# Kernel tuning notes

Hardware: AMD Instinct MI355X
Metric: run time of the kernel (lower is better)

The kernel has to match this reference:

```python
import jax, jax.numpy as jnp
import numpy as np

B, S, D = 4, 4096, 1024
H, DH = 16, 64            # heads, head dim (D = H*DH)
W = 256                   # local window size; S % W == 0
HID = 2 * D               # GEGLU hidden dim
LN_EPS = 1e-5


def setup_inputs() -> dict:
    key = jax.random.key(0)
    ks = jax.random.split(key, 8)
    w = lambda k, shp: (jax.random.normal(k, shp, jnp.float32) * 0.02)
    return {
        "x": jax.random.normal(ks[0], (B, S, D), jnp.float32),
        "ln1_g": jnp.ones((D,), jnp.float32), "ln1_b": jnp.zeros((D,), jnp.float32),
        "ln2_g": jnp.ones((D,), jnp.float32), "ln2_b": jnp.zeros((D,), jnp.float32),
        "Wq": w(ks[1], (D, D)), "Wk": w(ks[2], (D, D)), "Wv": w(ks[3], (D, D)),
        "Wo": w(ks[4], (D, D)), "bo": jnp.zeros((D,), jnp.float32),
        "W1": w(ks[5], (D, 2 * HID)), "b1": jnp.zeros((2 * HID,), jnp.float32),
        "W2": w(ks[6], (HID, D)), "b2": jnp.zeros((D,), jnp.float32),
    }


def layer_norm(x, g, b):
    mu = jnp.mean(x, axis=-1, keepdims=True)
    var = jnp.mean(jnp.square(x - mu), axis=-1, keepdims=True)
    return (x - mu) * jax.lax.rsqrt(var + LN_EPS) * g + b


def local_causal_attention(x, Wq, Wk, Wv, Wo, bo):
    b, s, d = x.shape
    nw = s // W
    def split_heads(t):  # [b,s,d] -> [b,H,nw,W,DH]
        return t.reshape(b, s, H, DH).transpose(0, 2, 1, 3).reshape(b, H, nw, W, DH)
    q = split_heads(x @ Wq)
    k = split_heads(x @ Wk)
    v = split_heads(x @ Wv)
    # look_backward=1: each window attends to [prev window, current window]
    def with_prev(t):  # [b,H,nw,W,DH] -> [b,H,nw,2W,DH]
        prev = jnp.pad(t, ((0, 0), (0, 0), (1, 0), (0, 0), (0, 0)))[:, :, :-1]
        return jnp.concatenate([prev, t], axis=3)
    kc, vc = with_prev(k), with_prev(v)
    scores = jnp.einsum("bhnqd,bhnkd->bhnqk", q, kc) * (DH ** -0.5)
    # positions: qpos = n*W + i ; kpos = (n-1)*W + j, j in [0,2W)
    n = jnp.arange(nw)[:, None, None]
    i = jnp.arange(W)[None, :, None]
    j = jnp.arange(2 * W)[None, None, :]
    qpos = n * W + i
    kpos = (n - 1) * W + j
    mask = (kpos <= qpos) & (kpos >= 0)  # causal + left-edge padding
    scores = jnp.where(mask[None, None], scores, jnp.finfo(scores.dtype).min)
    attn = jax.nn.softmax(scores, axis=-1)
    out = jnp.einsum("bhnqk,bhnkd->bhnqd", attn, vc)
    out = out.reshape(b, H, s, DH).transpose(0, 2, 1, 3).reshape(b, s, d)
    return out @ Wo + bo


def geglu(x, W1, b1, W2, b2):
    h = x @ W1 + b1
    a, g = jnp.split(h, 2, axis=-1)
    return (a * jax.nn.gelu(g, approximate=False)) @ W2 + b2


def reference(x, ln1_g, ln1_b, ln2_g, ln2_b, Wq, Wk, Wv, Wo, bo, W1, b1, W2, b2):
    x = x + local_causal_attention(layer_norm(x, ln1_g, ln1_b), Wq, Wk, Wv, Wo, bo)
    x = x + geglu(layer_norm(x, ln2_g, ln2_b), W1, b1, W2, b2)
    return x
```

## Files before the change

kernel.cpp:

```cpp
#include <hip/hip_runtime.h>
#include <hip/hip_bf16.h>

typedef __attribute__((ext_vector_type(4))) float f32x4;
typedef __attribute__((ext_vector_type(8))) short bf16x8;
typedef __attribute__((ext_vector_type(8))) unsigned short u16x8;

static __device__ __forceinline__ ushort f2b(float f) {
  union { float f; unsigned u; } v; v.f = f;
  unsigned r = v.u + 0x7fffu + ((v.u >> 16) & 1u);
  return (ushort)(r >> 16);
}

static __device__ __forceinline__ float gelu_fast(float g) {
  const float c0 = 0.7978845608028654f, c1 = 0.044715f;
  const float u = c0 * (g + c1 * g * g * g);
  const float e = __expf(2.0f * u);
  const float t = 1.0f - 2.0f / (e + 1.0f);
  return 0.5f * g * (1.0f + t);
}

static __device__ __forceinline__ void gload_lds16(const void* g, void* l) {
  __builtin_amdgcn_global_load_lds(
      (__attribute__((address_space(1))) void*)(g),
      (__attribute__((address_space(3))) void*)(l), 16, 0, 0);
}

__global__ __launch_bounds__(256) void transpose_cast_kernel(
    const float* __restrict__ W, ushort* __restrict__ Wt, int K, int N) {
  __shared__ float tile[32][33];
  const int n0 = blockIdx.x * 32, k0 = blockIdx.y * 32;
  const int tx = threadIdx.x, ty = threadIdx.y;
#pragma unroll
  for (int r = 0; r < 32; r += 8)
    tile[ty + r][tx] = W[(size_t)(k0 + ty + r) * N + n0 + tx];
  __syncthreads();
#pragma unroll
  for (int r = 0; r < 32; r += 8)
    Wt[(size_t)(n0 + ty + r) * K + k0 + tx] = f2b(tile[tx][ty + r]);
}

__global__ __launch_bounds__(256) void ln_kernel(
    const float* __restrict__ x, const float* __restrict__ g,
    const float* __restrict__ bb, ushort* __restrict__ out) {
  const int row = blockIdx.x;
  const float* xr = x + (size_t)row * 1024;
  const float4 v = *(const float4*)&xr[threadIdx.x * 4];
  float s = v.x + v.y + v.z + v.w;
  float s2 = v.x * v.x + v.y * v.y + v.z * v.z + v.w * v.w;
#pragma unroll
  for (int off = 32; off > 0; off >>= 1) {
    s += __shfl_down(s, off);
    s2 += __shfl_down(s2, off);
  }
  __shared__ float red[8];
  const int lane = threadIdx.x & 63, wv = threadIdx.x >> 6;
  if (lane == 0) { red[wv] = s; red[4 + wv] = s2; }
  __syncthreads();
  s = red[0] + red[1] + red[2] + red[3];
  s2 = red[4] + red[5] + red[6] + red[7];
  const float mu = s * (1.0f / 1024.0f);
  const float rs = rsqrtf(s2 * (1.0f / 1024.0f) - mu * mu + 1e-5f);
  const int c = threadIdx.x * 4;
  ushort4 o;
  o.x = f2b((v.x - mu) * rs * g[c + 0] + bb[c + 0]);
  o.y = f2b((v.y - mu) * rs * g[c + 1] + bb[c + 1]);
  o.z = f2b((v.z - mu) * rs * g[c + 2] + bb[c + 2]);
  o.w = f2b((v.w - mu) * rs * g[c + 3] + bb[c + 3]);
  *(ushort4*)&out[(size_t)row * 1024 + c] = o;
}

template <int MODE>
__global__ __launch_bounds__(512) void gemm256_kernel(
    const ushort* __restrict__ A, const ushort* __restrict__ Bt,
    const int M, const int N, const int K,
    ushort* __restrict__ Cb, float* __restrict__ Cf,
    const float* __restrict__ bias, const float* __restrict__ res) {
  __shared__ __align__(16) ushort lds[3 * 16384];

  const int ntn = N >> 8;
  const int bn = blockIdx.x % ntn;
  const int bm = blockIdx.x / ntn;
  const int tid = threadIdx.x;
  const int l = tid & 63, w = tid >> 6;
  const int wm = w >> 2, wn = w & 3;
  const int fr = l & 15, fq = l >> 4;

  const ushort* Ab = A + (size_t)bm * 256 * K;
  const ushort* Bb = Bt + (size_t)bn * 256 * K;

  const int srow = (l >> 2);
  const int scol = (((l & 3) ^ ((l >> 2) & 3)) * 8);

  f32x4 acc[8][4];
#pragma unroll
  for (int m = 0; m < 8; m++)
#pragma unroll
    for (int n = 0; n < 4; n++) acc[m][n] = (f32x4)0.0f;

  const int NT = K >> 5;

#define STAGE256(t)                                                            \
  {                                                                            \
    const int b3 = (t) % 3;                                                    \
    const size_t kk = (size_t)(t) * 32;                                        \
    _Pragma("unroll") for (int i = 0; i < 2; i++) {                            \
      const int r = (w * 2 + i) * 16 + srow;                                   \
      gload_lds16(Ab + (size_t)r * K + kk + scol,                              \
                  &lds[b3 * 16384 + (w * 2 + i) * 512]);                       \
      gload_lds16(Bb + (size_t)r * K + kk + scol,                              \
                  &lds[b3 * 16384 + 8192 + (w * 2 + i) * 512]);                \
    }                                                                          \
  }

  STAGE256(0);
  STAGE256(1);

  for (int t = 0; t < NT; ++t) {
    if (t + 2 < NT) {
      STAGE256(t + 2);
      asm volatile("s_waitcnt vmcnt(8)" ::: "memory");
    } else if (t + 1 < NT) {
      asm volatile("s_waitcnt vmcnt(4)" ::: "memory");
    } else {
      asm volatile("s_waitcnt vmcnt(0)" ::: "memory");
    }
    __builtin_amdgcn_s_barrier();
    asm volatile("" ::: "memory");

    const ushort* La = &lds[(t % 3) * 16384];
    const ushort* Lb = La + 8192;

    bf16x8 af[8], bf[4];
#pragma unroll
    for (int m = 0; m < 8; m++) {
      const int r = wm * 128 + m * 16 + fr;
      af[m] = *(const bf16x8*)&La[r * 32 + ((fq ^ (r & 3)) * 8)];
    }
#pragma unroll
    for (int n = 0; n < 4; n++) {
      const int r = wn * 64 + n * 16 + fr;
      bf[n] = *(const bf16x8*)&Lb[r * 32 + ((fq ^ (r & 3)) * 8)];
    }

    __builtin_amdgcn_s_setprio(1);
#pragma unroll
    for (int m = 0; m < 8; m++)
#pragma unroll
      for (int n = 0; n < 4; n++)
        acc[m][n] = __builtin_amdgcn_mfma_f32_16x16x32_bf16(af[m], bf[n], acc[m][n], 0, 0, 0);
    __builtin_amdgcn_s_setprio(0);

    asm volatile("" ::: "memory");
    __builtin_amdgcn_s_barrier();
  }
#undef STAGE256

  const int rowb = bm * 256 + wm * 128 + fq * 4;
  const int colb = bn * 256 + wn * 64 + fr;
#pragma unroll
  for (int m = 0; m < 8; m++) {
#pragma unroll
    for (int n = 0; n < 4; n++) {
      const int col = colb + n * 16;
#pragma unroll
      for (int j = 0; j < 4; j++) {
        const int row = rowb + m * 16 + j;
        float vv = acc[m][n][j];
        if (MODE == 0) {
          Cb[(size_t)row * N + col] = f2b(vv);
        } else if (MODE == 2) {
          if (col < 1024) vv *= 0.125f;
          Cb[(size_t)row * N + col] = f2b(vv);
        } else {
          Cf[(size_t)row * N + col] = vv + bias[col] + res[(size_t)row * N + col];
        }
      }
    }
  }
}

__global__ __launch_bounds__(256) void gemm_geglu_kernel(
    const ushort* __restrict__ A, const ushort* __restrict__ W1t,
    const float* __restrict__ b1, ushort* __restrict__ U) {
  const int K = 1024;
  __shared__ __align__(16) ushort lsA[128 * 32];
  __shared__ __align__(16) ushort lsBa[64 * 32];
  __shared__ __align__(16) ushort lsBg[64 * 32];
  const int bn = blockIdx.x & 31;
  const int bm = blockIdx.x >> 5;
  const int tid = threadIdx.x;
  const int lane = tid & 63, wv = tid >> 6;
  const int wr = wv >> 1, wc = wv & 1;
  const int fr = lane & 15, fq = lane >> 4;

  f32x4 acca[4][2], accg[4][2];
#pragma unroll
  for (int m = 0; m < 4; m++)
#pragma unroll
    for (int nn = 0; nn < 2; nn++) { acca[m][nn] = (f32x4)0.0f; accg[m][nn] = (f32x4)0.0f; }

  const ushort* Ab = A + (size_t)bm * 128 * K;
  const ushort* Bab = W1t + (size_t)bn * 64 * K;
  const ushort* Bgb = W1t + (size_t)(2048 + bn * 64) * K;
  const int r0 = tid >> 2;
  const int cseg = (tid & 3) * 8;

  for (int k0 = 0; k0 < K; k0 += 32) {
    gload_lds16(Ab + (size_t)r0 * K + (k0 + cseg), &lsA[wv * 512]);
    gload_lds16(Ab + (size_t)(r0 + 64) * K + (k0 + cseg), &lsA[wv * 512 + 2048]);
    gload_lds16(Bab + (size_t)r0 * K + (k0 + cseg), &lsBa[wv * 512]);
    gload_lds16(Bgb + (size_t)r0 * K + (k0 + cseg), &lsBg[wv * 512]);
    __syncthreads();
    bf16x8 af[4], ba[2], bg[2];
#pragma unroll
    for (int m = 0; m < 4; m++)
      af[m] = *(const bf16x8*)&lsA[(wr * 64 + m * 16 + fr) * 32 + fq * 8];
#pragma unroll
    for (int nn = 0; nn < 2; nn++) {
      ba[nn] = *(const bf16x8*)&lsBa[(wc * 32 + nn * 16 + fr) * 32 + fq * 8];
      bg[nn] = *(const bf16x8*)&lsBg[(wc * 32 + nn * 16 + fr) * 32 + fq * 8];
    }
#pragma unroll
    for (int m = 0; m < 4; m++)
#pragma unroll
      for (int nn = 0; nn < 2; nn++) {
        acca[m][nn] = __builtin_amdgcn_mfma_f32_16x16x32_bf16(af[m], ba[nn], acca[m][nn], 0, 0, 0);
        accg[m][nn] = __builtin_amdgcn_mfma_f32_16x16x32_bf16(af[m], bg[nn], accg[m][nn], 0, 0, 0);
      }
    __syncthreads();
  }

  const int rowb = bm * 128 + wr * 64 + fq * 4;
  const int colb = bn * 64 + wc * 32 + fr;
#pragma unroll
  for (int m = 0; m < 4; m++) {
#pragma unroll
    for (int nn = 0; nn < 2; nn++) {
      const int col = colb + nn * 16;
      const float b1a = b1[col];
      const float b1g = b1[2048 + col];
#pragma unroll
      for (int j = 0; j < 4; j++) {
        const int row = rowb + m * 16 + j;
        const float a = acca[m][nn][j] + b1a;
        const float gg = accg[m][nn][j] + b1g;
        U[(size_t)row * 2048 + col] = f2b(a * gelu_fast(gg));
      }
    }
  }
}

__global__ __launch_bounds__(256, 3) void attn_kernel(
    const ushort* __restrict__ Q, const ushort* __restrict__ Kb,
    const ushort* __restrict__ Vb, ushort* __restrict__ O, const int qs) {
  const int bx = blockIdx.x;
  const int n = bx & 15;
  const int h = (bx >> 4) & 15;
  const int b = bx >> 8;
  const int tid = threadIdx.x;
  const int lane = tid & 63, wv = tid >> 6;
  const int fr = lane & 15, fq = lane >> 4;

  __shared__ __align__(16) ushort Kl[64 * 72];
  __shared__ __align__(16) ushort Vt[64 * 70];
  __shared__ __align__(16) ushort Pl[4][64 * 68];

  const size_t qrow0 = (size_t)b * 4096 + (size_t)n * 256;

  bf16x8 qf[4][2];
#pragma unroll
  for (int m = 0; m < 4; m++)
#pragma unroll
    for (int kh = 0; kh < 2; kh++)
      qf[m][kh] = *(const bf16x8*)&Q[(qrow0 + wv * 64 + m * 16 + fr) * qs + h * 64 + kh * 32 + fq * 8];

  f32x4 oacc[4][4];
#pragma unroll
  for (int m = 0; m < 4; m++)
#pragma unroll
    for (int d = 0; d < 4; d++) oacc[m][d] = (f32x4)0.0f;

  float lsum[4][4];
#pragma unroll
  for (int m = 0; m < 4; m++)
#pragma unroll
    for (int j = 0; j < 4; j++) lsum[m][j] = 0.0f;

  const int c0 = (n == 0) ? 4 : 0;
  for (int c = c0; c < 8; c++) {
    const size_t kvrow0 =
        (size_t)((long long)b * 4096 + (long long)n * 256 + (long long)c * 64 - 256);
#pragma unroll
    for (int p = 0; p < 2; p++) {
      const int s = tid + p * 256;
      const int rr = s >> 3, cs2 = s & 7;
      *(u16x8*)&Kl[rr * 72 + cs2 * 8] =
          *(const u16x8*)&Kb[(kvrow0 + rr) * qs + h * 64 + cs2 * 8];
      const u16x8 vvv = *(const u16x8*)&Vb[(kvrow0 + rr) * qs + h * 64 + cs2 * 8];
#pragma unroll
      for (int i = 0; i < 8; i++) Vt[(cs2 * 8 + i) * 70 + rr] = vvv[i];
    }
    __syncthreads();

    if (c <= wv + 4) {
      const bool diag = (c == wv + 4);
#pragma unroll
      for (int nn = 0; nn < 4; nn++) {
        f32x4 sa[4];
#pragma unroll
        for (int m = 0; m < 4; m++) sa[m] = (f32x4)0.0f;
#pragma unroll
        for (int kh = 0; kh < 2; kh++) {
          const bf16x8 bk = *(const bf16x8*)&Kl[(nn * 16 + fr) * 72 + kh * 32 + fq * 8];
#pragma unroll
          for (int m = 0; m < 4; m++)
            sa[m] = __builtin_amdgcn_mfma_f32_16x16x32_bf16(qf[m][kh], bk, sa[m], 0, 0, 0);
        }
#pragma unroll
        for (int m = 0; m < 4; m++)
#pragma unroll
          for (int j = 0; j < 4; j++) {
            float p = __expf(sa[m][j]);
            if (diag && (nn * 16 + fr > m * 16 + fq * 4 + j)) p = 0.0f;
            lsum[m][j] += p;
            Pl[wv][(m * 16 + fq * 4 + j) * 68 + nn * 16 + fr] = f2b(p);
          }
      }
      __builtin_amdgcn_s_setprio(1);
#pragma unroll
      for (int kh = 0; kh < 2; kh++) {
        bf16x8 pa[4];
#pragma unroll
        for (int m = 0; m < 4; m++)
          pa[m] = *(const bf16x8*)&Pl[wv][(m * 16 + fr) * 68 + kh * 32 + fq * 8];
#pragma unroll
        for (int d = 0; d < 4; d++) {
          const bf16x8 vb = *(const bf16x8*)&Vt[(d * 16 + fr) * 70 + kh * 32 + fq * 8];
#pragma unroll
          for (int m = 0; m < 4; m++)
            oacc[m][d] = __builtin_amdgcn_mfma_f32_16x16x32_bf16(pa[m], vb, oacc[m][d], 0, 0, 0);
        }
      }
      __builtin_amdgcn_s_setprio(0);
    }
    __syncthreads();
  }

  float rl[4][4];
#pragma unroll
  for (int m = 0; m < 4; m++)
#pragma unroll
    for (int j = 0; j < 4; j++) {
      float t = lsum[m][j];
      t += __shfl_xor(t, 1);
      t += __shfl_xor(t, 2);
      t += __shfl_xor(t, 4);
      t += __shfl_xor(t, 8);
      rl[m][j] = 1.0f / t;
    }

#pragma unroll
  for (int m = 0; m < 4; m++)
#pragma unroll
    for (int d = 0; d < 4; d++)
#pragma unroll
      for (int j = 0; j < 4; j++) {
        const float o = oacc[m][d][j] * rl[m][j];
        O[(qrow0 + wv * 64 + m * 16 + fq * 4 + j) * 1024 + h * 64 + d * 16 + fr] = f2b(o);
      }
}

extern "C" void kernel_launch(void* const* d_in, const int* in_sizes, int n_in,
                              void* d_out, int out_size, void* d_ws, size_t ws_size,
                              hipStream_t stream) {
  (void)in_sizes; (void)n_in; (void)out_size; (void)ws_size;
  const float* x     = (const float*)d_in[0];
  const float* ln1_g = (const float*)d_in[1];
  const float* ln1_b = (const float*)d_in[2];
  const float* ln2_g = (const float*)d_in[3];
  const float* ln2_b = (const float*)d_in[4];
  const float* Wq    = (const float*)d_in[5];
  const float* Wk    = (const float*)d_in[6];
  const float* Wv    = (const float*)d_in[7];
  const float* Wo    = (const float*)d_in[8];
  const float* bo    = (const float*)d_in[9];
  const float* W1    = (const float*)d_in[10];
  const float* b1    = (const float*)d_in[11];
  const float* W2    = (const float*)d_in[12];
  const float* b2    = (const float*)d_in[13];

  char* ws = (char*)d_ws;
  const size_t MB = 1ull << 20;
  ushort* WQKVT = (ushort*)(ws + 0 * MB);
  ushort* WOT = (ushort*)(ws + 6 * MB);
  ushort* W1T = (ushort*)(ws + 8 * MB);
  ushort* W2T = (ushort*)(ws + 16 * MB);
  ushort* LN1 = (ushort*)(ws + 20 * MB);
  ushort* ATT = LN1;
  ushort* QKV = (ushort*)(ws + 52 * MB);
  ushort* LN2 = (ushort*)(ws + 52 * MB);
  ushort* U   = (ushort*)(ws + 84 * MB);
  float*  X1  = (float*)d_out;
  float*  OUT = (float*)d_out;

  const dim3 tb(32, 8);
  transpose_cast_kernel<<<dim3(32, 32), tb, 0, stream>>>(Wq, WQKVT, 1024, 1024);
  transpose_cast_kernel<<<dim3(32, 32), tb, 0, stream>>>(Wk, WQKVT + (size_t)1024 * 1024, 1024, 1024);
  transpose_cast_kernel<<<dim3(32, 32), tb, 0, stream>>>(Wv, WQKVT + (size_t)2048 * 1024, 1024, 1024);
  transpose_cast_kernel<<<dim3(32, 32), tb, 0, stream>>>(Wo, WOT, 1024, 1024);
  transpose_cast_kernel<<<dim3(128, 32), tb, 0, stream>>>(W1, W1T, 1024, 4096);
  transpose_cast_kernel<<<dim3(32, 64), tb, 0, stream>>>(W2, W2T, 2048, 1024);

  ln_kernel<<<16384, 256, 0, stream>>>(x, ln1_g, ln1_b, LN1);

  gemm256_kernel<2><<<64 * 12, 512, 0, stream>>>(LN1, WQKVT, 16384, 3072, 1024,
                                                 QKV, nullptr, nullptr, nullptr);

  attn_kernel<<<1024, 256, 0, stream>>>(QKV, QKV + 1024, QKV + 2048, ATT, 3072);

  gemm256_kernel<1><<<64 * 4, 512, 0, stream>>>(ATT, WOT, 16384, 1024, 1024,
                                                nullptr, X1, bo, x);

  ln_kernel<<<16384, 256, 0, stream>>>(X1, ln2_g, ln2_b, LN2);

  gemm_geglu_kernel<<<128 * 32, 256, 0, stream>>>(LN2, W1T, b1, U);

  gemm256_kernel<1><<<64 * 4, 512, 0, stream>>>(U, W2T, 16384, 1024, 2048,
                                                nullptr, OUT, b2, X1);
}
```

Baseline: 584.0 us.

## Rework GEGLU GEMM with larger tiles, triple-buffered LDS pipeline and swizzle

```diff
diff --git a/kernel.cpp b/kernel.cpp
--- a/kernel.cpp
+++ b/kernel.cpp
@@ -179,71 +179,112 @@
   }
 }
 
-__global__ __launch_bounds__(256) void gemm_geglu_kernel(
+__global__ __launch_bounds__(512) void gemm_geglu_kernel(
     const ushort* __restrict__ A, const ushort* __restrict__ W1t,
     const float* __restrict__ b1, ushort* __restrict__ U) {
   const int K = 1024;
-  __shared__ __align__(16) ushort lsA[128 * 32];
-  __shared__ __align__(16) ushort lsBa[64 * 32];
-  __shared__ __align__(16) ushort lsBg[64 * 32];
-  const int bn = blockIdx.x & 31;
-  const int bm = blockIdx.x >> 5;
+  __shared__ __align__(16) ushort lds[3 * 16384];
+
+  const int bn = blockIdx.x & 15;
+  const int bm = blockIdx.x >> 4;
   const int tid = threadIdx.x;
-  const int lane = tid & 63, wv = tid >> 6;
-  const int wr = wv >> 1, wc = wv & 1;
-  const int fr = lane & 15, fq = lane >> 4;
-
-  f32x4 acca[4][2], accg[4][2];
-#pragma unroll
-  for (int m = 0; m < 4; m++)
-#pragma unroll
-    for (int nn = 0; nn < 2; nn++) { acca[m][nn] = (f32x4)0.0f; accg[m][nn] = (f32x4)0.0f; }
-
-  const ushort* Ab = A + (size_t)bm * 128 * K;
-  const ushort* Bab = W1t + (size_t)bn * 64 * K;
-  const ushort* Bgb = W1t + (size_t)(2048 + bn * 64) * K;
-  const int r0 = tid >> 2;
-  const int cseg = (tid & 3) * 8;
-
-  for (int k0 = 0; k0 < K; k0 += 32) {
-    gload_lds16(Ab + (size_t)r0 * K + (k0 + cseg), &lsA[wv * 512]);
-    gload_lds16(Ab + (size_t)(r0 + 64) * K + (k0 + cseg), &lsA[wv * 512 + 2048]);
-    gload_lds16(Bab + (size_t)r0 * K + (k0 + cseg), &lsBa[wv * 512]);
-    gload_lds16(Bgb + (size_t)r0 * K + (k0 + cseg), &lsBg[wv * 512]);
-    __syncthreads();
-    bf16x8 af[4], ba[2], bg[2];
-#pragma unroll
-    for (int m = 0; m < 4; m++)
-      af[m] = *(const bf16x8*)&lsA[(wr * 64 + m * 16 + fr) * 32 + fq * 8];
-#pragma unroll
-    for (int nn = 0; nn < 2; nn++) {
-      ba[nn] = *(const bf16x8*)&lsBa[(wc * 32 + nn * 16 + fr) * 32 + fq * 8];
-      bg[nn] = *(const bf16x8*)&lsBg[(wc * 32 + nn * 16 + fr) * 32 + fq * 8];
-    }
-#pragma unroll
-    for (int m = 0; m < 4; m++)
-#pragma unroll
-      for (int nn = 0; nn < 2; nn++) {
-        acca[m][nn] = __builtin_amdgcn_mfma_f32_16x16x32_bf16(af[m], ba[nn], acca[m][nn], 0, 0, 0);
-        accg[m][nn] = __builtin_amdgcn_mfma_f32_16x16x32_bf16(af[m], bg[nn], accg[m][nn], 0, 0, 0);
-      }
-    __syncthreads();
-  }
-
-  const int rowb = bm * 128 + wr * 64 + fq * 4;
-  const int colb = bn * 64 + wc * 32 + fr;
-#pragma unroll
-  for (int m = 0; m < 4; m++) {
-#pragma unroll
-    for (int nn = 0; nn < 2; nn++) {
-      const int col = colb + nn * 16;
+  const int l = tid & 63, w = tid >> 6;
+  const int wm = w >> 2, wn = w & 3;
+  const int fr = l & 15, fq = l >> 4;
+
+  const ushort* Ab = A + (size_t)bm * 256 * K;
+  const ushort* Bab = W1t + (size_t)bn * 128 * K;
+  const ushort* Bgb = W1t + (size_t)(2048 + bn * 128) * K;
+
+  const int srow = (l >> 2);
+  const int scol = (((l & 3) ^ ((l >> 2) & 3)) * 8);
+  const int brow = (tid >> 2);
+  const int bscol = (((tid & 3) ^ ((tid >> 2) & 3)) * 8);
+
+  f32x4 acca[8][2], accg[8][2];
+#pragma unroll
+  for (int m = 0; m < 8; m++)
+#pragma unroll
+    for (int n = 0; n < 2; n++) { acca[m][n] = (f32x4)0.0f; accg[m][n] = (f32x4)0.0f; }
+
+  const int NT = K >> 5;
+
+#define STAGEGL(t)                                                             \
+  {                                                                            \
+    const int b3 = (t) % 3;                                                    \
+    const size_t kk = (size_t)(t) * 32;                                        \
+    _Pragma("unroll") for (int i = 0; i < 2; i++) {                            \
+      const int r = (w * 2 + i) * 16 + srow;                                   \
+      gload_lds16(Ab + (size_t)r * K + kk + scol,                              \
+                  &lds[b3 * 16384 + (w * 2 + i) * 512]);                       \
+    }                                                                          \
+    gload_lds16(Bab + (size_t)brow * K + kk + bscol,                           \
+                &lds[b3 * 16384 + 8192 + w * 512]);                            \
+    gload_lds16(Bgb + (size_t)brow * K + kk + bscol,                           \
+                &lds[b3 * 16384 + 12288 + w * 512]);                           \
+  }
+
+  STAGEGL(0);
+  STAGEGL(1);
+
+  for (int t = 0; t < NT; ++t) {
+    if (t + 2 < NT) {
+      STAGEGL(t + 2);
+      asm volatile("s_waitcnt vmcnt(8)" ::: "memory");
+    } else if (t + 1 < NT) {
+      asm volatile("s_waitcnt vmcnt(4)" ::: "memory");
+    } else {
+      asm volatile("s_waitcnt vmcnt(0)" ::: "memory");
+    }
+    __builtin_amdgcn_s_barrier();
+    asm volatile("" ::: "memory");
+
+    const ushort* La = &lds[(t % 3) * 16384];
+    const ushort* Lba = La + 8192;
+    const ushort* Lbg = La + 12288;
+
+    bf16x8 af[8], ba[2], bg[2];
+#pragma unroll
+    for (int m = 0; m < 8; m++) {
+      const int r = wm * 128 + m * 16 + fr;
+      af[m] = *(const bf16x8*)&La[r * 32 + ((fq ^ (r & 3)) * 8)];
+    }
+#pragma unroll
+    for (int n = 0; n < 2; n++) {
+      const int r = wn * 32 + n * 16 + fr;
+      ba[n] = *(const bf16x8*)&Lba[r * 32 + ((fq ^ (r & 3)) * 8)];
+      bg[n] = *(const bf16x8*)&Lbg[r * 32 + ((fq ^ (r & 3)) * 8)];
+    }
+
+    __builtin_amdgcn_s_setprio(1);
+#pragma unroll
+    for (int m = 0; m < 8; m++)
+#pragma unroll
+      for (int n = 0; n < 2; n++) {
+        acca[m][n] = __builtin_amdgcn_mfma_f32_16x16x32_bf16(af[m], ba[n], acca[m][n], 0, 0, 0);
+        accg[m][n] = __builtin_amdgcn_mfma_f32_16x16x32_bf16(af[m], bg[n], accg[m][n], 0, 0, 0);
+      }
+    __builtin_amdgcn_s_setprio(0);
+
+    asm volatile("" ::: "memory");
+    __builtin_amdgcn_s_barrier();
+  }
+#undef STAGEGL
+
+  const int rowb = bm * 256 + wm * 128 + fq * 4;
+  const int colb = bn * 128 + wn * 32 + fr;
+#pragma unroll
+  for (int m = 0; m < 8; m++) {
+#pragma unroll
+    for (int n = 0; n < 2; n++) {
+      const int col = colb + n * 16;
       const float b1a = b1[col];
       const float b1g = b1[2048 + col];
 #pragma unroll
       for (int j = 0; j < 4; j++) {
         const int row = rowb + m * 16 + j;
-        const float a = acca[m][nn][j] + b1a;
-        const float gg = accg[m][nn][j] + b1g;
+        const float a = acca[m][n][j] + b1a;
+        const float gg = accg[m][n][j] + b1g;
         U[(size_t)row * 2048 + col] = f2b(a * gelu_fast(gg));
       }
     }
@@ -423,7 +464,7 @@
 
   ln_kernel<<<16384, 256, 0, stream>>>(X1, ln2_g, ln2_b, LN2);
 
-  gemm_geglu_kernel<<<128 * 32, 256, 0, stream>>>(LN2, W1T, b1, U);
+  gemm_geglu_kernel<<<64 * 16, 512, 0, stream>>>(LN2, W1T, b1, U);
 
   gemm256_kernel<1><<<64 * 4, 512, 0, stream>>>(U, W2T, 16384, 1024, 2048,
                                                 nullptr, OUT, b2, X1);
```

New measurement: 573.8 us. No clear change (-1.8%).
